# Optimization experiments

Hardware: AMD Instinct MI355X
Metric: run time of the kernel (lower is better)

## Reference

```python
import jax, jax.numpy as jnp
import numpy as np

N = 8192        # total nodes in the batch of graphs
E = 262144      # edges (avg degree 32)
F_IN = 128      # input node features
G = 64          # graphs in batch
C = 10          # classes
K1, K2, K3 = 4096, 2048, 1024  # int(0.5*N), int(0.5*K1), int(0.5*K2)


def setup_inputs() -> dict:
    key = jax.random.key(0)
    ks = jax.random.split(key, 16)
    def lin(k, i, o):
        return jax.random.normal(k, (i, o), jnp.float32) / np.float32(np.sqrt(i))
    return {
        "x": jax.random.normal(ks[0], (N, F_IN), jnp.float32),
        "edge_index": jax.random.randint(ks[1], (2, E), 0, N),
        "batch": jnp.sort(jax.random.randint(ks[2], (N,), 0, G)),
        "W1": lin(ks[3], F_IN, 32), "b1": jnp.zeros((32,), jnp.float32),
        "W2": lin(ks[4], 32, 64),   "b2": jnp.zeros((64,), jnp.float32),
        "W3": lin(ks[5], 64, 128),  "b3": jnp.zeros((128,), jnp.float32),
        "W4": lin(ks[6], 128, 256), "b4": jnp.zeros((256,), jnp.float32),
        "W5": lin(ks[7], 384, 128), "b5": jnp.zeros((128,), jnp.float32),
        "W6": lin(ks[8], 192, 64),  "b6": jnp.zeros((64,), jnp.float32),
        "W7": lin(ks[9], 96, 32),   "b7": jnp.zeros((32,), jnp.float32),
        "p1": jax.random.normal(ks[10], (32,), jnp.float32),
        "p2": jax.random.normal(ks[11], (64,), jnp.float32),
        "p3": jax.random.normal(ks[12], (128,), jnp.float32),
        "Wl1": lin(ks[13], 64, 64),
        "Wc": lin(ks[14], 64, C), "bc": jnp.zeros((C,), jnp.float32),
    }


def _gcn(A, x, W, b):
    # PyG GCNConv (improved=False): out = D^-1/2 (A+I) D^-1/2 propagated src->dst.
    n = A.shape[0]
    Ah = A + jnp.eye(n, dtype=A.dtype)
    deg = Ah.sum(axis=0)                                  # degree at targets (cols)
    dinv = jnp.where(deg > 0, deg ** -0.5, 0.0).astype(A.dtype)
    An = dinv[:, None] * Ah * dinv[None, :]               # edge norm d[src]^-.5 * d[dst]^-.5
    return An.T @ (x @ W) + b                             # out[dst] += norm * (xW)[src]


def _gpool(A, x, p, k):
    # GPool: scores = Linear(x)/||p||, top-k select, gate by sigmoid, reindex dense adj.
    scores = (x @ p) / jnp.linalg.norm(p)                 # [n]
    vals, idx = jax.lax.top_k(scores, k)
    xp = x[idx] * jax.nn.sigmoid(vals)[:, None]
    Ap = (A[idx][:, idx] > 0).astype(x.dtype)             # dense_to_sparse rebinarizes
    return xp, Ap, idx


def reference(x, edge_index, batch, W1, b1, W2, b2, W3, b3, W4, b4, W5, b5,
              W6, b6, W7, b7, p1, p2, p3, Wl1, Wc, bc):
    elu = jax.nn.elu
    # to_dense_adj: dense N x N adjacency (duplicate edges accumulate)
    A = jnp.zeros((N, N), x.dtype).at[edge_index[0], edge_index[1]].add(1.0)
    x1 = elu(_gcn(A, x, W1, b1))
    x2, A2, i2 = _gpool(A, x1, p1, K1); x2 = elu(x2)
    x3 = elu(_gcn(A2, x2, W2, b2))
    x4, A4, i4 = _gpool(A2, x3, p2, K2); x4 = elu(x4)
    x5 = elu(_gcn(A4, x4, W3, b3))
    x6, A6, i6 = _gpool(A4, x5, p3, K3); x6 = elu(x6)
    x7 = elu(_gcn(A6, x6, W4, b4))
    u = jnp.zeros((K2, x7.shape[1]), x7.dtype).at[i6].set(x7)   # GUnpool
    x8 = elu(jnp.concatenate([u, x5], axis=1))
    x9 = elu(_gcn(A4, x8, W5, b5))
    u = jnp.zeros((K1, x9.shape[1]), x9.dtype).at[i4].set(x9)
    x10 = elu(jnp.concatenate([u, x3], axis=1))
    x11 = elu(_gcn(A2, x10, W6, b6))
    u = jnp.zeros((N, x11.shape[1]), x11.dtype).at[i2].set(x11)
    x12 = elu(jnp.concatenate([u, x1], axis=1))
    x13 = elu(_gcn(A, x12, W7, b7))
    gmax = jax.ops.segment_max(x13, batch, num_segments=G)      # global max pool
    gsum = jax.ops.segment_sum(x13, batch, num_segments=G)
    cnt = jax.ops.segment_sum(jnp.ones((N, 1), x13.dtype), batch, num_segments=G)
    h = elu(jnp.concatenate([gmax, gsum / cnt], axis=1))        # [G, 64]
    h = elu(h @ Wl1)
    return jax.nn.log_softmax(h @ Wc + bc, axis=-1)
```

## Files before the change

### kernel.cpp

```cpp
#include <hip/hip_runtime.h>
#include <math.h>

#define NN 8192
#define EE 262144
#define GG 64
#define CC 10
#define KK1 4096
#define KK2 2048
#define KK3 1024
#define PITCH 128

typedef unsigned long long ull;

__device__ __forceinline__ float eluf(float x) { return x > 0.f ? x : expm1f(x); }
__device__ __forceinline__ float sigf(float x) { return 1.f / (1.f + expf(-x)); }
__device__ __forceinline__ unsigned f2s(float f) {
    unsigned u = __float_as_uint(f);
    return (u & 0x80000000u) ? ~u : (u | 0x80000000u);
}

__global__ void k_init(const int* __restrict__ ei, unsigned* __restrict__ bitmap,
                       int* __restrict__ cnt1, int* __restrict__ csr1,
                       const int* __restrict__ batch, int* __restrict__ gstart,
                       const float* __restrict__ X, const float* __restrict__ W,
                       float* __restrict__ Y) {
    __shared__ float Xs[32][33];
    __shared__ float Ws[32][36];
    int tid = threadIdx.x;
    if ((int)blockIdx.x >= 1024) {
        int txn = tid & 7, tym = tid >> 3;
        int m0 = ((int)blockIdx.x - 1024) * 32;
        float4 acc = make_float4(0.f, 0.f, 0.f, 0.f);
        for (int k0 = 0; k0 < 128; k0 += 32) {
            int r = tid >> 3, c4 = (tid & 7) << 2;
            *(float4*)&Xs[r][c4] = *(const float4*)&X[(size_t)(m0 + r) * 128 + k0 + c4];
            *(float4*)&Ws[r][c4] = *(const float4*)&W[(size_t)(k0 + r) * 32 + c4];
            __syncthreads();
#pragma unroll 8
            for (int kk = 0; kk < 32; kk++) {
                float4 wv = *(const float4*)&Ws[kk][txn * 4];
                float xv = Xs[tym][kk];
                acc.x += xv * wv.x; acc.y += xv * wv.y;
                acc.z += xv * wv.z; acc.w += xv * wv.w;
            }
            __syncthreads();
        }
        *(float4*)&Y[(size_t)(m0 + tym) * 32 + txn * 4] = acc;
        return;
    }
    int e = blockIdx.x * 256 + tid;
    int s = ei[e], d = ei[EE + e];
    unsigned key = ((unsigned)s << 13) | (unsigned)d;
    unsigned old = atomicOr(&bitmap[key >> 5], 1u << (key & 31u));
    int dup = (old >> (key & 31u)) & 1;
    int pos = atomicAdd(&cnt1[d], 1);
    csr1[(d << 7) + pos] = dup ? (s | 0x80000000) : s;
    if (e < NN) {
        int g = batch[e];
        int prev = (e == 0) ? -1 : batch[e - 1];
        for (int gg = prev + 1; gg <= g; gg++) gstart[gg] = e;
        if (e == NN - 1)
            for (int gg = g + 1; gg <= GG; gg++) gstart[gg] = NN;
    }
}

__global__ void k_dinv1(const int* __restrict__ cnt, float* __restrict__ dinv) {
    int j = blockIdx.x * 256 + threadIdx.x;
    dinv[j] = 1.f / sqrtf((float)(cnt[j] + 1));
}

template<int L1>
__global__ void k_pool_sub(const float* __restrict__ x, const float* __restrict__ score,
                           const int* __restrict__ idx, int k, int F,
                           float* __restrict__ xout, int nPool,
                           const int* __restrict__ csrP, const int* __restrict__ roffP,
                           const int* __restrict__ degP,
                           const int* __restrict__ invmap,
                           int* __restrict__ csrO, int* __restrict__ roffO,
                           int* __restrict__ degO, float* __restrict__ dinvO) {
    if ((int)blockIdx.x < nPool) {
        int t = blockIdx.x * 256 + threadIdx.x;
        if (t >= k * F) return;
        int r = t / F, f = t - r * F;
        int j = idx[r];
        xout[t] = eluf(x[(size_t)j * F + f] * sigf(score[j]));
        return;
    }
    int wid = (((int)blockIdx.x - nPool) * 256 + (int)threadIdx.x) >> 6;
    int lane = threadIdx.x & 63;
    if (wid >= k) return;
    int j = idx[wid];
    int j0 = L1 ? (j << 7) : roffP[j];
    int len = degP[j];
    int cnt = 0;
    for (int base = 0; base < len; base += 64) {
        bool sel = false;
        int val = 0;
        if (base + lane < len) {
            int e = csrP[j0 + base + lane];
            if (!L1 || e >= 0) {
                int s = L1 ? (e & 0x7fffffff) : e;
                int v = invmap[s];
                if (v >= 0) { sel = true; val = v; }
            }
        }
        ull m = __ballot(sel);
        if (sel) {
            int off = __popcll(m & ((1ull << lane) - 1ull));
            csrO[j0 + cnt + off] = val;
        }
        cnt += __popcll(m);
    }
    if (lane == 0) {
        roffO[wid] = j0;
        degO[wid] = cnt;
        dinvO[wid] = 1.f / sqrtf((float)(cnt + 1));
    }
}

__global__ void k_gemm(const float* __restrict__ X, const float* __restrict__ W,
                       float* __restrict__ Y, int M, int K, int F) {
    __shared__ float Xs[32][33];
    __shared__ float Ws[32][36];
    int tid = threadIdx.x;
    int txn = tid & 7, tym = tid >> 3;
    int m0 = blockIdx.x * 32, n0 = blockIdx.y * 32;
    float4 acc = make_float4(0.f, 0.f, 0.f, 0.f);
    for (int k0 = 0; k0 < K; k0 += 32) {
        {
            int r = tid >> 3, c4 = (tid & 7) << 2;
            *(float4*)&Xs[r][c4] = *(const float4*)&X[(size_t)(m0 + r) * K + k0 + c4];
            *(float4*)&Ws[r][c4] = *(const float4*)&W[(size_t)(k0 + r) * F + n0 + c4];
        }
        __syncthreads();
#pragma unroll 8
        for (int kk = 0; kk < 32; kk++) {
            float4 wv = *(const float4*)&Ws[kk][txn * 4];
            float xv = Xs[tym][kk];
            acc.x += xv * wv.x; acc.y += xv * wv.y;
            acc.z += xv * wv.z; acc.w += xv * wv.w;
        }
        __syncthreads();
    }
    *(float4*)&Y[(size_t)(m0 + tym) * F + n0 + txn * 4] = acc;
}

__global__ void k_gemm_up(const float* __restrict__ xl, const int* __restrict__ inv,
                          const float* __restrict__ xr, int Fl, int Fr,
                          const float* __restrict__ W, float* __restrict__ Y,
                          int M, int K, int F) {
    __shared__ float Xs[32][33];
    __shared__ float Ws[32][36];
    __shared__ int sIdx[32];
    int tid = threadIdx.x;
    int txn = tid & 7, tym = tid >> 3;
    int m0 = blockIdx.x * 32, n0 = blockIdx.y * 32;
    if (tid < 32) sIdx[tid] = inv[m0 + tid];
    float4 acc = make_float4(0.f, 0.f, 0.f, 0.f);
    __syncthreads();
    for (int k0 = 0; k0 < K; k0 += 32) {
        {
            int r = tid >> 3, c4 = (tid & 7) << 2;
            int kk = k0 + c4;
            float4 v;
            if (kk < Fl) {
                int rr = sIdx[r];
                v = (rr >= 0) ? *(const float4*)&xl[(size_t)rr * Fl + kk]
                              : make_float4(0.f, 0.f, 0.f, 0.f);
            } else {
                v = *(const float4*)&xr[(size_t)(m0 + r) * Fr + (kk - Fl)];
            }
            v.x = eluf(v.x); v.y = eluf(v.y); v.z = eluf(v.z); v.w = eluf(v.w);
            *(float4*)&Xs[r][c4] = v;
            *(float4*)&Ws[r][c4] = *(const float4*)&W[(size_t)(k0 + r) * F + n0 + c4];
        }
        __syncthreads();
#pragma unroll 8
        for (int kk = 0; kk < 32; kk++) {
            float4 wv = *(const float4*)&Ws[kk][txn * 4];
            float xv = Xs[tym][kk];
            acc.x += xv * wv.x; acc.y += xv * wv.y;
            acc.z += xv * wv.z; acc.w += xv * wv.w;
        }
        __syncthreads();
    }
    *(float4*)&Y[(size_t)(m0 + tym) * F + n0 + txn * 4] = acc;
}

template<int LOGF, int SCORE, int L1>
__global__ void k_prop(const int* __restrict__ csr, const int* __restrict__ roff,
                       const int* __restrict__ deg, const float* __restrict__ dinv,
                       const float* __restrict__ xW, const float* __restrict__ b,
                       float* __restrict__ xout, const float* __restrict__ p,
                       float* __restrict__ score) {
    constexpr int FQ = 1 << (LOGF - 2);
    const float4* xW4 = (const float4*)xW;
    int t = blockIdx.x * 256 + threadIdx.x;
    int d = t >> (LOGF - 2), q = t & (FQ - 1);
    int j0 = L1 ? (d << 7) : roff[d];
    int j1 = j0 + deg[d];
    float dd = dinv[d];
    float4 v0 = xW4[t];
    float4 sum = make_float4(dd * v0.x, dd * v0.y, dd * v0.z, dd * v0.w);
    for (int j = j0; j < j1; j++) {
        int e = csr[j];
        int s = L1 ? (e & 0x7fffffff) : e;
        float ds = dinv[s];
        float4 xv = xW4[(s << (LOGF - 2)) + q];
        sum.x += ds * xv.x; sum.y += ds * xv.y;
        sum.z += ds * xv.z; sum.w += ds * xv.w;
    }
    float4 bv = *(const float4*)&b[q << 2];
    float4 o;
    o.x = eluf(dd * sum.x + bv.x);
    o.y = eluf(dd * sum.y + bv.y);
    o.z = eluf(dd * sum.z + bv.z);
    o.w = eluf(dd * sum.w + bv.w);
    ((float4*)xout)[t] = o;
    if (SCORE) {
        float4 pv = *(const float4*)&p[q << 2];
        float sc = o.x * pv.x + o.y * pv.y + o.z * pv.z + o.w * pv.w;
        float nr = pv.x * pv.x + pv.y * pv.y + pv.z * pv.z + pv.w * pv.w;
#pragma unroll
        for (int m = FQ >> 1; m >= 1; m >>= 1) {
            sc += __shfl_xor(sc, m, 64);
            nr += __shfl_xor(nr, m, 64);
        }
        if (q == 0) score[d] = sc / sqrtf(nr);
    }
}

__device__ __forceinline__ ull cex_shfl(ull v, int st, bool takeMax) {
    ull pv = __shfl_xor(v, st, 64);
    return takeMax ? (v > pv ? v : pv) : (v < pv ? v : pv);
}
__device__ __forceinline__ void cexr(ull& a, ull& b, bool desc) {
    if (desc ? (a < b) : (a > b)) { ull x = a; a = b; b = x; }
}

__global__ void k_wsort(const float* __restrict__ score, ull* __restrict__ keys,
                        int last, int k, int* __restrict__ out_idx,
                        int* __restrict__ invmap) {
    __shared__ ull sk[2048];
    int tid = threadIdx.x;
    int base = blockIdx.x << 11;
    int giA = base + tid, giB = giA + 1024;
    ull a = ((ull)f2s(score[giA]) << 32) | (unsigned)(~giA);
    ull b = ((ull)f2s(score[giB]) << 32) | (unsigned)(~giB);
    for (int sz = 2; sz <= 2048; sz <<= 1) {
        int st = sz >> 1;
        if (st >= 64) {
            sk[tid] = a; sk[tid + 1024] = b;
            __syncthreads();
            for (; st >= 64; st >>= 1) {
                int i = ((tid & ~(st - 1)) << 1) | (tid & (st - 1));
                int j = i | st;
                ull u = sk[i], v = sk[j];
                bool desc = (((base + i) & sz) == 0);
                if (desc ? (u < v) : (u > v)) { sk[i] = v; sk[j] = u; }
                __syncthreads();
            }
            a = sk[tid]; b = sk[tid + 1024];
        }
        for (; st >= 1; st >>= 1) {
            bool low = (tid & st) == 0;
            bool descA = ((giA & sz) == 0);
            bool descB = ((giB & sz) == 0);
            a = cex_shfl(a, st, descA == low);
            b = cex_shfl(b, st, descB == low);
        }
    }
    if (last) {
        if (giA < k) {
            int j = (int)(~(unsigned)(a & 0xFFFFFFFFu));
            out_idx[giA] = j; invmap[j] = giA;
        }
        if (giB < k) {
            int j = (int)(~(unsigned)(b & 0xFFFFFFFFu));
            out_idx[giB] = j; invmap[j] = giB;
        }
    } else {
        keys[giA] = a; keys[giB] = b;
    }
}

__global__ void k_stage4k_m(ull* __restrict__ keys) {
    __shared__ ull sk[4096];
    int tid = threadIdx.x;
    int base = blockIdx.x << 12;
    bool desc = ((base & 4096) == 0);
    ull k0 = keys[base + tid], k1 = keys[base + tid + 1024];
    ull k2 = keys[base + tid + 2048], k3 = keys[base + tid + 3072];
    cexr(k0, k2, desc); cexr(k1, k3, desc);
    sk[tid] = k0; sk[tid + 1024] = k1; sk[tid + 2048] = k2; sk[tid + 3072] = k3;
    __syncthreads();
    for (int st = 1024; st >= 64; st >>= 1) {
        for (int pp = tid; pp < 2048; pp += 1024) {
            int i = ((pp & ~(st - 1)) << 1) | (pp & (st - 1));
            int j = i | st;
            ull u = sk[i], v = sk[j];
            if (desc ? (u < v) : (u > v)) { sk[i] = v; sk[j] = u; }
        }
        __syncthreads();
    }
    k0 = sk[tid]; k1 = sk[tid + 1024]; k2 = sk[tid + 2048]; k3 = sk[tid + 3072];
    for (int st = 32; st >= 1; st >>= 1) {
        bool low = (tid & st) == 0;
        k0 = cex_shfl(k0, st, desc == low);
        k1 = cex_shfl(k1, st, desc == low);
        k2 = cex_shfl(k2, st, desc == low);
        k3 = cex_shfl(k3, st, desc == low);
    }
    keys[base + tid] = k0; keys[base + tid + 1024] = k1;
    keys[base + tid + 2048] = k2; keys[base + tid + 3072] = k3;
}

__global__ void k_stage8k_f(const ull* __restrict__ keys, int* __restrict__ out_idx,
                            int* __restrict__ invmap) {
    __shared__ ull sk[4096];
    int tid = threadIdx.x;
    ull a0 = keys[tid],        a1 = keys[tid + 1024];
    ull a2 = keys[tid + 2048], a3 = keys[tid + 3072];
    ull b0 = keys[tid + 4096], b1 = keys[tid + 5120];
    ull b2 = keys[tid + 6144], b3 = keys[tid + 7168];
    cexr(a0, b0, true); cexr(a1, b1, true);
    cexr(a2, b2, true); cexr(a3, b3, true);
    cexr(a0, a2, true); cexr(a1, a3, true);
    sk[tid] = a0; sk[tid + 1024] = a1; sk[tid + 2048] = a2; sk[tid + 3072] = a3;
    __syncthreads();
    for (int st = 1024; st >= 64; st >>= 1) {
        for (int pp = tid; pp < 2048; pp += 1024) {
            int i = ((pp & ~(st - 1)) << 1) | (pp & (st - 1));
            int j = i | st;
            ull u = sk[i], v = sk[j];
            if (u < v) { sk[i] = v; sk[j] = u; }
        }
        __syncthreads();
    }
    a0 = sk[tid]; a1 = sk[tid + 1024]; a2 = sk[tid + 2048]; a3 = sk[tid + 3072];
    for (int st = 32; st >= 1; st >>= 1) {
        bool low = (tid & st) == 0;
        a0 = cex_shfl(a0, st, low);
        a1 = cex_shfl(a1, st, low);
        a2 = cex_shfl(a2, st, low);
        a3 = cex_shfl(a3, st, low);
    }
    int p, j;
    p = tid;        j = (int)(~(unsigned)(a0 & 0xFFFFFFFFu)); out_idx[p] = j; invmap[j] = p;
    p = tid + 1024; j = (int)(~(unsigned)(a1 & 0xFFFFFFFFu)); out_idx[p] = j; invmap[j] = p;
    p = tid + 2048; j = (int)(~(unsigned)(a2 & 0xFFFFFFFFu)); out_idx[p] = j; invmap[j] = p;
    p = tid + 3072; j = (int)(~(unsigned)(a3 & 0xFFFFFFFFu)); out_idx[p] = j; invmap[j] = p;
}

__global__ void k_stage4k_f(const ull* __restrict__ keys, int* __restrict__ out_idx,
                            int* __restrict__ invmap) {
    __shared__ ull sk[2048];
    int tid = threadIdx.x;
    ull a0 = keys[tid],        a1 = keys[tid + 1024];
    ull a2 = keys[tid + 2048], a3 = keys[tid + 3072];
    cexr(a0, a2, true); cexr(a1, a3, true);
    sk[tid] = a0; sk[tid + 1024] = a1;
    __syncthreads();
    for (int st = 1024; st >= 64; st >>= 1) {
        int i = ((tid & ~(st - 1)) << 1) | (tid & (st - 1));
        int j = i | st;
        ull u = sk[i], v = sk[j];
        if (u < v) { sk[i] = v; sk[j] = u; }
        __syncthreads();
    }
    a0 = sk[tid]; a1 = sk[tid + 1024];
    for (int st = 32; st >= 1; st >>= 1) {
        bool low = (tid & st) == 0;
        a0 = cex_shfl(a0, st, low);
        a1 = cex_shfl(a1, st, low);
    }
    int p, j;
    p = tid;        j = (int)(~(unsigned)(a0 & 0xFFFFFFFFu)); out_idx[p] = j; invmap[j] = p;
    p = tid + 1024; j = (int)(~(unsigned)(a1 & 0xFFFFFFFFu)); out_idx[p] = j; invmap[j] = p;
}

__global__ void k_seg2(const float* __restrict__ x13, const int* __restrict__ gstart,
                       float* __restrict__ gmaxf, float* __restrict__ gsum,
                       int* __restrict__ gcnt) {
    __shared__ float sm[8][32], ss[8][32];
    int g = blockIdx.x;
    int j0 = gstart[g], j1 = gstart[g + 1];
    int t = threadIdx.x;
    int f = t & 31, r = t >> 5;
    float m = -INFINITY, s = 0.f;
    for (int j = j0 + r; j < j1; j += 8) {
        float v = x13[(j << 5) + f];
        m = fmaxf(m, v);
        s += v;
    }
    sm[r][f] = m; ss[r][f] = s;
    __syncthreads();
    if (t < 32) {
        float mm = sm[0][t], sss = ss[0][t];
        for (int i = 1; i < 8; i++) { mm = fmaxf(mm, sm[i][t]); sss += ss[i][t]; }
        gmaxf[(g << 5) + t] = mm;
        gsum[(g << 5) + t] = sss;
        if (t == 0) gcnt[g] = j1 - j0;
    }
}

__global__ void k_head(const float* __restrict__ gmaxf, const float* __restrict__ gsum,
                       const int* __restrict__ gcnt, const float* __restrict__ Wl1,
                       const float* __restrict__ Wc, const float* __restrict__ bc,
                       float* __restrict__ out) {
    __shared__ float h0[GG * 64];
    __shared__ float h1[GG * 64];
    __shared__ float lg[GG * CC];
    int tid = threadIdx.x;
    for (int t = tid; t < GG * 64; t += blockDim.x) {
        int g = t >> 6, c = t & 63;
        float v;
        if (c < 32) v = gmaxf[(g << 5) + c];
        else v = gsum[(g << 5) + (c - 32)] / (float)gcnt[g];
        h0[t] = eluf(v);
    }
    __syncthreads();
    for (int t = tid; t < GG * 64; t += blockDim.x) {
        int g = t >> 6, j = t & 63;
        float s = 0.f;
        for (int k = 0; k < 64; k++) s += h0[(g << 6) + k] * Wl1[k * 64 + j];
        h1[t] = eluf(s);
    }
    __syncthreads();
    for (int t = tid; t < GG * CC; t += blockDim.x) {
        int g = t / CC, c = t - g * CC;
        float s = bc[c];
        for (int k = 0; k < 64; k++) s += h1[(g << 6) + k] * Wc[k * CC + c];
        lg[t] = s;
    }
    __syncthreads();
    if (tid < GG) {
        int g = tid;
        float m = -1e30f;
        for (int c = 0; c < CC; c++) m = fmaxf(m, lg[g * CC + c]);
        float se = 0.f;
        for (int c = 0; c < CC; c++) se += expf(lg[g * CC + c] - m);
        float lse = m + logf(se);
        for (int c = 0; c < CC; c++) out[g * CC + c] = lg[g * CC + c] - lse;
    }
}

static void run_topk(const float* score, ull* keys, int n, int k, int* out_idx,
                     int* invmap, hipStream_t stream) {
    if (n == 2048) {
        k_wsort<<<1, 1024, 0, stream>>>(score, keys, 1, k, out_idx, invmap);
    } else if (n == 4096) {
        k_wsort<<<2, 1024, 0, stream>>>(score, keys, 0, k, out_idx, invmap);
        k_stage4k_f<<<1, 1024, 0, stream>>>(keys, out_idx, invmap);
    } else {
        k_wsort<<<4, 1024, 0, stream>>>(score, keys, 0, k, out_idx, invmap);
        k_stage4k_m<<<2, 1024, 0, stream>>>(keys);
        k_stage8k_f<<<1, 1024, 0, stream>>>(keys, out_idx, invmap);
    }
}

extern "C" void kernel_launch(void* const* d_in, const int* in_sizes, int n_in,
                              void* d_out, int out_size, void* d_ws, size_t ws_size,
                              hipStream_t stream) {
    const float* x = (const float*)d_in[0];
    const int* ei = (const int*)d_in[1];
    const int* batch = (const int*)d_in[2];
    const float* W1 = (const float*)d_in[3];  const float* b1 = (const float*)d_in[4];
    const float* W2 = (const float*)d_in[5];  const float* b2 = (const float*)d_in[6];
    const float* W3 = (const float*)d_in[7];  const float* b3 = (const float*)d_in[8];
    const float* W4 = (const float*)d_in[9];  const float* b4 = (const float*)d_in[10];
    const float* W5 = (const float*)d_in[11]; const float* b5 = (const float*)d_in[12];
    const float* W6 = (const float*)d_in[13]; const float* b6 = (const float*)d_in[14];
    const float* W7 = (const float*)d_in[15]; const float* b7 = (const float*)d_in[16];
    const float* p1 = (const float*)d_in[17];
    const float* p2 = (const float*)d_in[18];
    const float* p3 = (const float*)d_in[19];
    const float* Wl1 = (const float*)d_in[20];
    const float* Wc = (const float*)d_in[21];
    const float* bc = (const float*)d_in[22];
    float* out = (float*)d_out;
    (void)in_sizes; (void)n_in; (void)out_size; (void)ws_size;

    char* w = (char*)d_ws;
    size_t off = 0;
    auto alloc = [&](size_t bytes) -> char* {
        char* p = w + off;
        off = (off + bytes + 255) & ~(size_t)255;
        return p;
    };

    size_t zero_begin = off;
    unsigned* bitmap = (unsigned*)alloc((size_t)NN * NN / 8);
    int* cnt1 = (int*)alloc(NN * 4);
    size_t zero_len = off - zero_begin;

    size_t ff_begin = off;
    int* pos2 = (int*)alloc(NN * 4);
    int* inv4 = (int*)alloc(KK1 * 4);
    int* inv6 = (int*)alloc(KK2 * 4);
    size_t ff_len = off - ff_begin;

    float* dinv1 = (float*)alloc(NN * 4);
    float* dinv2 = (float*)alloc(KK1 * 4);
    float* dinv3 = (float*)alloc(KK2 * 4);
    float* dinv4 = (float*)alloc(KK3 * 4);
    int* roff2 = (int*)alloc(KK1 * 4); int* deg2 = (int*)alloc(KK1 * 4);
    int* roff3 = (int*)alloc(KK2 * 4); int* deg3 = (int*)alloc(KK2 * 4);
    int* roff4 = (int*)alloc(KK3 * 4); int* deg4 = (int*)alloc(KK3 * 4);
    int* csr1 = (int*)alloc((size_t)NN * PITCH * 4);
    int* csr2 = (int*)alloc((size_t)NN * PITCH * 4);
    int* csr3 = (int*)alloc((size_t)NN * PITCH * 4);
    int* csr4 = (int*)alloc((size_t)NN * PITCH * 4);
    float* xW = (float*)alloc((size_t)262144 * 4);
    float* x1 = (float*)alloc((size_t)NN * 32 * 4);
    float* x2 = (float*)alloc((size_t)KK1 * 32 * 4);
    float* x3 = (float*)alloc((size_t)KK1 * 64 * 4);
    float* x4 = (float*)alloc((size_t)KK2 * 64 * 4);
    float* x5 = (float*)alloc((size_t)KK2 * 128 * 4);
    float* x6 = (float*)alloc((size_t)KK3 * 128 * 4);
    float* x7 = (float*)alloc((size_t)KK3 * 256 * 4);
    float* x9 = (float*)alloc((size_t)KK2 * 128 * 4);
    float* x11 = (float*)alloc((size_t)KK1 * 64 * 4);
    float* x13 = (float*)alloc((size_t)NN * 32 * 4);
    float* score1 = (float*)alloc(NN * 4);
    float* score2 = (float*)alloc(KK1 * 4);
    float* score3 = (float*)alloc(KK2 * 4);
    int* i2 = (int*)alloc(KK1 * 4);
    int* i4 = (int*)alloc(KK2 * 4);
    int* i6 = (int*)alloc(KK3 * 4);
    ull* keys = (ull*)alloc((size_t)NN * 8);
    int* gstart = (int*)alloc((GG + 1) * 4);
    float* gmaxf = (float*)alloc(GG * 32 * 4);
    float* gsum = (float*)alloc(GG * 32 * 4);
    int* gcnt = (int*)alloc(GG * 4);

    hipMemsetAsync(w + zero_begin, 0, zero_len, stream);
    hipMemsetAsync(w + ff_begin, 0xFF, ff_len, stream);

    const int B = 256;
    k_init<<<1280, B, 0, stream>>>(ei, bitmap, cnt1, csr1, batch, gstart, x, W1, xW);
    k_dinv1<<<32, B, 0, stream>>>(cnt1, dinv1);

    k_prop<5, 1, 1><<<(NN * 8) / B, B, 0, stream>>>(csr1, nullptr, cnt1, dinv1, xW, b1,
                                                    x1, p1, score1);

    run_topk(score1, keys, NN, KK1, i2, pos2, stream);
    k_pool_sub<1><<<512 + KK1 / 4, B, 0, stream>>>(x1, score1, i2, KK1, 32, x2, 512,
                                                   csr1, nullptr, cnt1, pos2,
                                                   csr2, roff2, deg2, dinv2);

    k_gemm<<<dim3(KK1 / 32, 2), B, 0, stream>>>(x2, W2, xW, KK1, 32, 64);
    k_prop<6, 1, 0><<<(KK1 * 16) / B, B, 0, stream>>>(csr2, roff2, deg2, dinv2, xW, b2,
                                                      x3, p2, score2);

    run_topk(score2, keys, KK1, KK2, i4, inv4, stream);
    k_pool_sub<0><<<512 + KK2 / 4, B, 0, stream>>>(x3, score2, i4, KK2, 64, x4, 512,
                                                   csr2, roff2, deg2, inv4,
                                                   csr3, roff3, deg3, dinv3);

    k_gemm<<<dim3(KK2 / 32, 4), B, 0, stream>>>(x4, W3, xW, KK2, 64, 128);
    k_prop<7, 1, 0><<<(KK2 * 32) / B, B, 0, stream>>>(csr3, roff3, deg3, dinv3, xW, b3,
                                                      x5, p3, score3);

    run_topk(score3, keys, KK2, KK3, i6, inv6, stream);
    k_pool_sub<0><<<512 + KK3 / 4, B, 0, stream>>>(x5, score3, i6, KK3, 128, x6, 512,
                                                   csr3, roff3, deg3, inv6,
                                                   csr4, roff4, deg4, dinv4);

    k_gemm<<<dim3(KK3 / 32, 8), B, 0, stream>>>(x6, W4, xW, KK3, 128, 256);
    k_prop<8, 0, 0><<<(KK3 * 64) / B, B, 0, stream>>>(csr4, roff4, deg4, dinv4, xW, b4,
                                                      x7, nullptr, nullptr);

    k_gemm_up<<<dim3(KK2 / 32, 4), B, 0, stream>>>(x7, inv6, x5, 256, 128,
                                                   W5, xW, KK2, 384, 128);
    k_prop<7, 0, 0><<<(KK2 * 32) / B, B, 0, stream>>>(csr3, roff3, deg3, dinv3, xW, b5,
                                                      x9, nullptr, nullptr);

    k_gemm_up<<<dim3(KK1 / 32, 2), B, 0, stream>>>(x9, inv4, x3, 128, 64,
                                                   W6, xW, KK1, 192, 64);
    k_prop<6, 0, 0><<<(KK1 * 16) / B, B, 0, stream>>>(csr2, roff2, deg2, dinv2, xW, b6,
                                                      x11, nullptr, nullptr);

    k_gemm_up<<<dim3(NN / 32, 1), B, 0, stream>>>(x11, pos2, x1, 64, 32,
                                                  W7, xW, NN, 96, 32);
    k_prop<5, 0, 1><<<(NN * 8) / B, B, 0, stream>>>(csr1, nullptr, cnt1, dinv1, xW, b7,
                                                    x13, nullptr, nullptr);

    k_seg2<<<GG, B, 0, stream>>>(x13, gstart, gmaxf, gsum, gcnt);
    k_head<<<1, 1024, 0, stream>>>(gmaxf, gsum, gcnt, Wl1, Wc, bc, out);
}
```

Baseline: 367.9 us.

## Split GCN neighbor loops across lanes and drop dinv1 kernel and 0xFF memset

Each GCN propagation now assigns S lanes per (node, feature-quad) and strides the edge list across them, combining the partial sums with xor shuffles, so more threads are in flight and per-thread edge chains are shorter. The level-1 degree normalisation is computed inline from the degree counts, which removes the separate dinv1 kernel. The inverse index maps now store index+1, so they can share the zero memset and the 0xFF memset is no longer needed. The cost is extra shuffle reductions, recomputing rsqrt per edge at level 1, and redundant epilogue work on the non-leader lanes.

```diff
diff --git a/kernel.cpp b/kernel.cpp
--- a/kernel.cpp
+++ b/kernel.cpp
@@ -64,11 +64,6 @@
     }
 }
 
-__global__ void k_dinv1(const int* __restrict__ cnt, float* __restrict__ dinv) {
-    int j = blockIdx.x * 256 + threadIdx.x;
-    dinv[j] = 1.f / sqrtf((float)(cnt[j] + 1));
-}
-
 template<int L1>
 __global__ void k_pool_sub(const float* __restrict__ x, const float* __restrict__ score,
                            const int* __restrict__ idx, int k, int F,
@@ -101,7 +96,7 @@
             if (!L1 || e >= 0) {
                 int s = L1 ? (e & 0x7fffffff) : e;
                 int v = invmap[s];
-                if (v >= 0) { sel = true; val = v; }
+                if (v > 0) { sel = true; val = v - 1; }
             }
         }
         ull m = __ballot(sel);
@@ -165,8 +160,8 @@
             float4 v;
             if (kk < Fl) {
                 int rr = sIdx[r];
-                v = (rr >= 0) ? *(const float4*)&xl[(size_t)rr * Fl + kk]
-                              : make_float4(0.f, 0.f, 0.f, 0.f);
+                v = (rr > 0) ? *(const float4*)&xl[(size_t)(rr - 1) * Fl + kk]
+                             : make_float4(0.f, 0.f, 0.f, 0.f);
             } else {
                 v = *(const float4*)&xr[(size_t)(m0 + r) * Fr + (kk - Fl)];
             }
@@ -187,28 +182,46 @@
     *(float4*)&Y[(size_t)(m0 + tym) * F + n0 + txn * 4] = acc;
 }
 
-template<int LOGF, int SCORE, int L1>
+template<int LOGF, int SCORE, int L1, int LS>
 __global__ void k_prop(const int* __restrict__ csr, const int* __restrict__ roff,
                        const int* __restrict__ deg, const float* __restrict__ dinv,
                        const float* __restrict__ xW, const float* __restrict__ b,
                        float* __restrict__ xout, const float* __restrict__ p,
                        float* __restrict__ score) {
     constexpr int FQ = 1 << (LOGF - 2);
+    constexpr int S = 1 << LS;
+    constexpr int RL = FQ * S;
     const float4* xW4 = (const float4*)xW;
     int t = blockIdx.x * 256 + threadIdx.x;
-    int d = t >> (LOGF - 2), q = t & (FQ - 1);
+    int d = t >> (LOGF - 2 + LS);
+    int rem = t & (RL - 1);
+    int q = rem >> LS, h = rem & (S - 1);
     int j0 = L1 ? (d << 7) : roff[d];
-    int j1 = j0 + deg[d];
-    float dd = dinv[d];
-    float4 v0 = xW4[t];
-    float4 sum = make_float4(dd * v0.x, dd * v0.y, dd * v0.z, dd * v0.w);
-    for (int j = j0; j < j1; j++) {
+    int dg = deg[d];
+    int j1 = j0 + dg;
+    float dd = L1 ? (1.f / sqrtf((float)(dg + 1))) : dinv[d];
+    int idx = (d << (LOGF - 2)) + q;
+    float4 sum;
+    if (h == 0) {
+        float4 v0 = xW4[idx];
+        sum = make_float4(dd * v0.x, dd * v0.y, dd * v0.z, dd * v0.w);
+    } else {
+        sum = make_float4(0.f, 0.f, 0.f, 0.f);
+    }
+    for (int j = j0 + h; j < j1; j += S) {
         int e = csr[j];
         int s = L1 ? (e & 0x7fffffff) : e;
-        float ds = dinv[s];
+        float ds = L1 ? (1.f / sqrtf((float)(deg[s] + 1))) : dinv[s];
         float4 xv = xW4[(s << (LOGF - 2)) + q];
         sum.x += ds * xv.x; sum.y += ds * xv.y;
         sum.z += ds * xv.z; sum.w += ds * xv.w;
+    }
+#pragma unroll
+    for (int m = 1; m < S; m <<= 1) {
+        sum.x += __shfl_xor(sum.x, m, 64);
+        sum.y += __shfl_xor(sum.y, m, 64);
+        sum.z += __shfl_xor(sum.z, m, 64);
+        sum.w += __shfl_xor(sum.w, m, 64);
     }
     float4 bv = *(const float4*)&b[q << 2];
     float4 o;
@@ -216,17 +229,20 @@
     o.y = eluf(dd * sum.y + bv.y);
     o.z = eluf(dd * sum.z + bv.z);
     o.w = eluf(dd * sum.w + bv.w);
-    ((float4*)xout)[t] = o;
+    if (h == 0) ((float4*)xout)[idx] = o;
     if (SCORE) {
         float4 pv = *(const float4*)&p[q << 2];
-        float sc = o.x * pv.x + o.y * pv.y + o.z * pv.z + o.w * pv.w;
-        float nr = pv.x * pv.x + pv.y * pv.y + pv.z * pv.z + pv.w * pv.w;
+        float sc = 0.f, nr = 0.f;
+        if (h == 0) {
+            sc = o.x * pv.x + o.y * pv.y + o.z * pv.z + o.w * pv.w;
+            nr = pv.x * pv.x + pv.y * pv.y + pv.z * pv.z + pv.w * pv.w;
+        }
 #pragma unroll
-        for (int m = FQ >> 1; m >= 1; m >>= 1) {
+        for (int m = RL >> 1; m >= 1; m >>= 1) {
             sc += __shfl_xor(sc, m, 64);
             nr += __shfl_xor(nr, m, 64);
         }
-        if (q == 0) score[d] = sc / sqrtf(nr);
+        if (rem == 0) score[d] = sc / sqrtf(nr);
     }
 }
 
@@ -273,11 +289,11 @@
     if (last) {
         if (giA < k) {
             int j = (int)(~(unsigned)(a & 0xFFFFFFFFu));
-            out_idx[giA] = j; invmap[j] = giA;
+            out_idx[giA] = j; invmap[j] = giA + 1;
         }
         if (giB < k) {
             int j = (int)(~(unsigned)(b & 0xFFFFFFFFu));
-            out_idx[giB] = j; invmap[j] = giB;
+            out_idx[giB] = j; invmap[j] = giB + 1;
         }
     } else {
         keys[giA] = a; keys[giB] = b;
@@ -346,10 +362,10 @@
         a3 = cex_shfl(a3, st, low);
     }
     int p, j;
-    p = tid;        j = (int)(~(unsigned)(a0 & 0xFFFFFFFFu)); out_idx[p] = j; invmap[j] = p;
-    p = tid + 1024; j = (int)(~(unsigned)(a1 & 0xFFFFFFFFu)); out_idx[p] = j; invmap[j] = p;
-    p = tid + 2048; j = (int)(~(unsigned)(a2 & 0xFFFFFFFFu)); out_idx[p] = j; invmap[j] = p;
-    p = tid + 3072; j = (int)(~(unsigned)(a3 & 0xFFFFFFFFu)); out_idx[p] = j; invmap[j] = p;
+    p = tid;        j = (int)(~(unsigned)(a0 & 0xFFFFFFFFu)); out_idx[p] = j; invmap[j] = p + 1;
+    p = tid + 1024; j = (int)(~(unsigned)(a1 & 0xFFFFFFFFu)); out_idx[p] = j; invmap[j] = p + 1;
+    p = tid + 2048; j = (int)(~(unsigned)(a2 & 0xFFFFFFFFu)); out_idx[p] = j; invmap[j] = p + 1;
+    p = tid + 3072; j = (int)(~(unsigned)(a3 & 0xFFFFFFFFu)); out_idx[p] = j; invmap[j] = p + 1;
 }
 
 __global__ void k_stage4k_f(const ull* __restrict__ keys, int* __restrict__ out_idx,
@@ -375,8 +391,8 @@
         a1 = cex_shfl(a1, st, low);
     }
     int p, j;
-    p = tid;        j = (int)(~(unsigned)(a0 & 0xFFFFFFFFu)); out_idx[p] = j; invmap[j] = p;
-    p = tid + 1024; j = (int)(~(unsigned)(a1 & 0xFFFFFFFFu)); out_idx[p] = j; invmap[j] = p;
+    p = tid;        j = (int)(~(unsigned)(a0 & 0xFFFFFFFFu)); out_idx[p] = j; invmap[j] = p + 1;
+    p = tid + 1024; j = (int)(~(unsigned)(a1 & 0xFFFFFFFFu)); out_idx[p] = j; invmap[j] = p + 1;
 }
 
 __global__ void k_seg2(const float* __restrict__ x13, const int* __restrict__ gstart,
@@ -492,15 +508,11 @@
     size_t zero_begin = off;
     unsigned* bitmap = (unsigned*)alloc((size_t)NN * NN / 8);
     int* cnt1 = (int*)alloc(NN * 4);
-    size_t zero_len = off - zero_begin;
-
-    size_t ff_begin = off;
     int* pos2 = (int*)alloc(NN * 4);
     int* inv4 = (int*)alloc(KK1 * 4);
     int* inv6 = (int*)alloc(KK2 * 4);
-    size_t ff_len = off - ff_begin;
-
-    float* dinv1 = (float*)alloc(NN * 4);
+    size_t zero_len = off - zero_begin;
+
     float* dinv2 = (float*)alloc(KK1 * 4);
     float* dinv3 = (float*)alloc(KK2 * 4);
     float* dinv4 = (float*)alloc(KK3 * 4);
@@ -535,14 +547,12 @@
     int* gcnt = (int*)alloc(GG * 4);
 
     hipMemsetAsync(w + zero_begin, 0, zero_len, stream);
-    hipMemsetAsync(w + ff_begin, 0xFF, ff_len, stream);
 
     const int B = 256;
     k_init<<<1280, B, 0, stream>>>(ei, bitmap, cnt1, csr1, batch, gstart, x, W1, xW);
-    k_dinv1<<<32, B, 0, stream>>>(cnt1, dinv1);
-
-    k_prop<5, 1, 1><<<(NN * 8) / B, B, 0, stream>>>(csr1, nullptr, cnt1, dinv1, xW, b1,
-                                                    x1, p1, score1);
+
+    k_prop<5, 1, 1, 3><<<2048, B, 0, stream>>>(csr1, nullptr, cnt1, nullptr, xW, b1,
+                                               x1, p1, score1);
 
     run_topk(score1, keys, NN, KK1, i2, pos2, stream);
     k_pool_sub<1><<<512 + KK1 / 4, B, 0, stream>>>(x1, score1, i2, KK1, 32, x2, 512,
@@ -550,8 +560,8 @@
                                                    csr2, roff2, deg2, dinv2);
 
     k_gemm<<<dim3(KK1 / 32, 2), B, 0, stream>>>(x2, W2, xW, KK1, 32, 64);
-    k_prop<6, 1, 0><<<(KK1 * 16) / B, B, 0, stream>>>(csr2, roff2, deg2, dinv2, xW, b2,
-                                                      x3, p2, score2);
+    k_prop<6, 1, 0, 2><<<1024, B, 0, stream>>>(csr2, roff2, deg2, dinv2, xW, b2,
+                                               x3, p2, score2);
 
     run_topk(score2, keys, KK1, KK2, i4, inv4, stream);
     k_pool_sub<0><<<512 + KK2 / 4, B, 0, stream>>>(x3, score2, i4, KK2, 64, x4, 512,
@@ -559,8 +569,8 @@
                                                    csr3, roff3, deg3, dinv3);
 
     k_gemm<<<dim3(KK2 / 32, 4), B, 0, stream>>>(x4, W3, xW, KK2, 64, 128);
-    k_prop<7, 1, 0><<<(KK2 * 32) / B, B, 0, stream>>>(csr3, roff3, deg3, dinv3, xW, b3,
-                                                      x5, p3, score3);
+    k_prop<7, 1, 0, 1><<<512, B, 0, stream>>>(csr3, roff3, deg3, dinv3, xW, b3,
+                                              x5, p3, score3);
 
     run_topk(score3, keys, KK2, KK3, i6, inv6, stream);
     k_pool_sub<0><<<512 + KK3 / 4, B, 0, stream>>>(x5, score3, i6, KK3, 128, x6, 512,
@@ -568,23 +578,23 @@
                                                    csr4, roff4, deg4, dinv4);
 
     k_gemm<<<dim3(KK3 / 32, 8), B, 0, stream>>>(x6, W4, xW, KK3, 128, 256);
-    k_prop<8, 0, 0><<<(KK3 * 64) / B, B, 0, stream>>>(csr4, roff4, deg4, dinv4, xW, b4,
-                                                      x7, nullptr, nullptr);
+    k_prop<8, 0, 0, 1><<<512, B, 0, stream>>>(csr4, roff4, deg4, dinv4, xW, b4,
+                                              x7, nullptr, nullptr);
 
     k_gemm_up<<<dim3(KK2 / 32, 4), B, 0, stream>>>(x7, inv6, x5, 256, 128,
                                                    W5, xW, KK2, 384, 128);
-    k_prop<7, 0, 0><<<(KK2 * 32) / B, B, 0, stream>>>(csr3, roff3, deg3, dinv3, xW, b5,
-                                                      x9, nullptr, nullptr);
+    k_prop<7, 0, 0, 2><<<1024, B, 0, stream>>>(csr3, roff3, deg3, dinv3, xW, b5,
+                                               x9, nullptr, nullptr);
 
     k_gemm_up<<<dim3(KK1 / 32, 2), B, 0, stream>>>(x9, inv4, x3, 128, 64,
                                                    W6, xW, KK1, 192, 64);
-    k_prop<6, 0, 0><<<(KK1 * 16) / B, B, 0, stream>>>(csr2, roff2, deg2, dinv2, xW, b6,
-                                                      x11, nullptr, nullptr);
+    k_prop<6, 0, 0, 2><<<1024, B, 0, stream>>>(csr2, roff2, deg2, dinv2, xW, b6,
+                                               x11, nullptr, nullptr);
 
     k_gemm_up<<<dim3(NN / 32, 1), B, 0, stream>>>(x11, pos2, x1, 64, 32,
                                                   W7, xW, NN, 96, 32);
-    k_prop<5, 0, 1><<<(NN * 8) / B, B, 0, stream>>>(csr1, nullptr, cnt1, dinv1, xW, b7,
-                                                    x13, nullptr, nullptr);
+    k_prop<5, 0, 1, 3><<<2048, B, 0, stream>>>(csr1, nullptr, cnt1, nullptr, xW, b7,
+                                               x13, nullptr, nullptr);
 
     k_seg2<<<GG, B, 0, stream>>>(x13, gstart, gmaxf, gsum, gcnt);
     k_head<<<1, 1024, 0, stream>>>(gmaxf, gsum, gcnt, Wl1, Wc, bc, out);
```

Measured after the change: 333.4 us. 1.1x faster.
